# Kernel tuning notes

Hardware: AMD Instinct MI355X
Metric: run time of the kernel (lower is better)

The kernel has to match this reference:

```python
import jax, jax.numpy as jnp
import numpy as np

CROP_H, CROP_W = 14, 14


def _crop_and_resize_one_image(img, nboxes):
    """TF tf.image.crop_and_resize (bilinear, extrapolation_value=0) for one image.

    img: [H, W, C] float; nboxes: [N, 4] normalized (y1, x1, y2, x2).
    Returns [N, CROP_H, CROP_W, C].
    """
    H, W, C = img.shape
    dt = img.dtype
    y1, x1, y2, x2 = nboxes[:, 0], nboxes[:, 1], nboxes[:, 2], nboxes[:, 3]

    # Sample grid in pixel coordinates (crop size > 1 branch of TF op).
    ty = jnp.arange(CROP_H, dtype=dt) / (CROP_H - 1)  # [ch]
    tx = jnp.arange(CROP_W, dtype=dt) / (CROP_W - 1)  # [cw]
    ys = (y1[:, None] + (y2 - y1)[:, None] * ty[None, :]) * (H - 1)  # [N, ch]
    xs = (x1[:, None] + (x2 - x1)[:, None] * tx[None, :]) * (W - 1)  # [N, cw]

    valid_y = (ys >= 0) & (ys <= H - 1)  # [N, ch]
    valid_x = (xs >= 0) & (xs <= W - 1)  # [N, cw]

    y0f = jnp.floor(ys)
    x0f = jnp.floor(xs)
    wy = ys - y0f  # [N, ch]
    wx = xs - x0f  # [N, cw]
    y0 = jnp.clip(y0f, 0, H - 1).astype(jnp.int32)
    y1i = jnp.clip(y0f + 1, 0, H - 1).astype(jnp.int32)
    x0 = jnp.clip(x0f, 0, W - 1).astype(jnp.int32)
    x1i = jnp.clip(x0f + 1, 0, W - 1).astype(jnp.int32)

    def gather(yi, xi):  # yi [N,ch], xi [N,cw] -> [N,ch,cw,C]
        return img[yi[:, :, None], xi[:, None, :]]

    tl = gather(y0, x0)
    tr = gather(y0, x1i)
    bl = gather(y1i, x0)
    br = gather(y1i, x1i)

    wy_ = wy[:, :, None, None]
    wx_ = wx[:, None, :, None]
    out = (tl * (1 - wy_) * (1 - wx_) + tr * (1 - wy_) * wx_
           + bl * wy_ * (1 - wx_) + br * wy_ * wx_)

    mask = (valid_y[:, :, None] & valid_x[:, None, :])[..., None]
    return jnp.where(mask, out, jnp.zeros((), dtype=dt))


def setup_inputs() -> dict:
    key = jax.random.key(0)
    k1, k2, k3, k4, k5, k6 = jax.random.split(key, 6)
    B, N, H, W, C = 4, 256, 256, 256, 256
    # Boxes in pixel coordinates [x1, y1, x2, y2] with 0 <= x1 < x2 <= W etc.
    x1 = jax.random.uniform(k1, (B, N), minval=0.0, maxval=W / 2)
    y1 = jax.random.uniform(k2, (B, N), minval=0.0, maxval=H / 2)
    bw = jax.random.uniform(k3, (B, N), minval=4.0, maxval=W / 2)
    bh = jax.random.uniform(k4, (B, N), minval=4.0, maxval=H / 2)
    boxes = jnp.stack([x1, y1, x1 + bw, y1 + bh], axis=-1).astype(jnp.float32)
    fpn = jax.random.normal(k5, (B, H, W, C), dtype=jnp.float32)
    return {"boxes": boxes, "fpn": fpn}


def reference(boxes, fpn):
    boxes = jax.lax.stop_gradient(boxes)
    fpn = jax.lax.stop_gradient(fpn)
    B, H, W, C = fpn.shape
    Hf = jnp.asarray(H, dtype=fpn.dtype)
    Wf = jnp.asarray(W, dtype=fpn.dtype)

    x1 = boxes[..., 0]
    y1 = boxes[..., 1]
    x2 = boxes[..., 2]
    y2 = boxes[..., 3]
    # Exact normalization from the layer (image_shape == per-sample fpn shape).
    ny1 = y1 / Hf * Hf / (Hf - 1)
    nx1 = x1 / Wf * Wf / (Wf - 1)
    ny2 = (y2 / Hf * Hf - 1) / (Hf - 1)
    nx2 = (x2 / Wf * Wf - 1) / (Wf - 1)
    norm_boxes = jnp.stack([ny1, nx1, ny2, nx2], axis=-1)  # [B, N, 4]

    return jax.vmap(_crop_and_resize_one_image)(fpn, norm_boxes)
```

## Files before the change

### kernel.cpp

```cpp
#include <hip/hip_runtime.h>

constexpr int CROP_H = 14;
constexpr int CROP_W = 14;
constexpr int B = 4, N = 256, H = 256, W = 256, C = 256;
constexpr int C4 = C / 4;
constexpr int POSITIONS = B * N * CROP_H * CROP_W;
constexpr int NBOXES = B * N;
constexpr int ITEMS = NBOXES * CROP_H;
constexpr int NBINS = B * H;
constexpr int NXCD = 8;
constexpr int POS_PER_XCD = POSITIONS / NXCD;
constexpr size_t WS_NEEDED_BYTES = (size_t)ITEMS * 4;

typedef float vfloat4 __attribute__((ext_vector_type(4)));

__global__ __launch_bounds__(1024) void sort_rows_kernel(
    const float* __restrict__ boxes, unsigned int* __restrict__ perm) {
  __shared__ unsigned int cnt[NBINS];
  __shared__ unsigned int wsum[16];
  const int tid = threadIdx.x;
  cnt[tid] = 0u;
  __syncthreads();

  const float* bx = boxes + (size_t)tid * 4;
  const float y1 = bx[1], y2 = bx[3];
  const float Hf = (float)H;
  const float ny1 = y1 / Hf * Hf / (Hf - 1.0f);
  const float ny2 = (y2 / Hf * Hf - 1.0f) / (Hf - 1.0f);
  const int bimg = tid >> 8;

  unsigned int mybin[CROP_H];
#pragma unroll
  for (int i = 0; i < CROP_H; ++i) {
    float ty = (float)i / (float)(CROP_H - 1);
    float ys = (ny1 + (ny2 - ny1) * ty) * (Hf - 1.0f);
    float y0f = floorf(ys);
    int y0 = (int)fminf(fmaxf(y0f, 0.0f), Hf - 1.0f);
    mybin[i] = ((unsigned)bimg << 8) | (unsigned)y0;
    atomicAdd(&cnt[mybin[i]], 1u);
  }
  __syncthreads();

  unsigned c0 = cnt[tid];
  unsigned v = c0;
#pragma unroll
  for (int d = 1; d < 64; d <<= 1) {
    unsigned u = __shfl_up(v, d);
    if ((tid & 63) >= d) v += u;
  }
  if ((tid & 63) == 63) wsum[tid >> 6] = v;
  __syncthreads();
  if (tid == 0) {
    unsigned acc = 0;
    for (int w = 0; w < 16; ++w) { unsigned t = wsum[w]; wsum[w] = acc; acc += t; }
  }
  __syncthreads();
  cnt[tid] = v - c0 + wsum[tid >> 6];
  __syncthreads();

#pragma unroll
  for (int i = 0; i < CROP_H; ++i) {
    unsigned slot = atomicAdd(&cnt[mybin[i]], 1u);
    perm[slot] = (unsigned)(tid * CROP_H + i);
  }
}

template <bool USE_PERM>
__global__ __launch_bounds__(256) void roi_align_kernel(
    const float* __restrict__ boxes,
    const float* __restrict__ fpn,
    float* __restrict__ out,
    const unsigned int* __restrict__ perm) {
  const int wave = threadIdx.x >> 6;
  const int lane = threadIdx.x & 63;

  int pos;
  if (USE_PERM) {
    const int xcd = blockIdx.x & 7;
    const int r   = blockIdx.x >> 3;
    const unsigned slot = (unsigned)(xcd * POS_PER_XCD + r * 4 + wave);
    const unsigned it = slot / 14u;
    const unsigned jj = slot - it * 14u;
    pos = (int)(perm[it] * 14u + jj);
  } else {
    pos = blockIdx.x * 4 + wave;
  }

  int j = pos % CROP_W;
  int t = pos / CROP_W;
  int i = t % CROP_H;
  t /= CROP_H;
  int n = t % N;
  int b = t / N;

  const float* bx = boxes + (size_t)(b * N + n) * 4;
  float x1 = bx[0], y1 = bx[1], x2 = bx[2], y2 = bx[3];

  const float Hf = (float)H, Wf = (float)W;
  float ny1 = y1 / Hf * Hf / (Hf - 1.0f);
  float nx1 = x1 / Wf * Wf / (Wf - 1.0f);
  float ny2 = (y2 / Hf * Hf - 1.0f) / (Hf - 1.0f);
  float nx2 = (x2 / Wf * Wf - 1.0f) / (Wf - 1.0f);

  float ty = (float)i / (float)(CROP_H - 1);
  float tx = (float)j / (float)(CROP_W - 1);
  float ys = (ny1 + (ny2 - ny1) * ty) * (Hf - 1.0f);
  float xs = (nx1 + (nx2 - nx1) * tx) * (Wf - 1.0f);

  bool valid = (ys >= 0.0f) && (ys <= Hf - 1.0f) &&
               (xs >= 0.0f) && (xs <= Wf - 1.0f);

  float y0f = floorf(ys), x0f = floorf(xs);
  float wy = ys - y0f, wx = xs - x0f;
  int y0  = (int)fminf(fmaxf(y0f,        0.0f), Hf - 1.0f);
  int y1i = (int)fminf(fmaxf(y0f + 1.0f, 0.0f), Hf - 1.0f);
  int x0  = (int)fminf(fmaxf(x0f,        0.0f), Wf - 1.0f);
  int x1i = (int)fminf(fmaxf(x0f + 1.0f, 0.0f), Wf - 1.0f);

  const float4* f4 = (const float4*)fpn;
  int rb = b * H;
  size_t i00 = (size_t)((rb + y0)  * W + x0)  * C4 + lane;
  size_t i01 = (size_t)((rb + y0)  * W + x1i) * C4 + lane;
  size_t i10 = (size_t)((rb + y1i) * W + x0)  * C4 + lane;
  size_t i11 = (size_t)((rb + y1i) * W + x1i) * C4 + lane;

  float4 tl = f4[i00];
  float4 tr = f4[i01];
  float4 bl = f4[i10];
  float4 br = f4[i11];

  float w00 = (1.0f - wy) * (1.0f - wx);
  float w01 = (1.0f - wy) * wx;
  float w10 = wy * (1.0f - wx);
  float w11 = wy * wx;

  vfloat4 o;
  o.x = tl.x * w00 + tr.x * w01 + bl.x * w10 + br.x * w11;
  o.y = tl.y * w00 + tr.y * w01 + bl.y * w10 + br.y * w11;
  o.z = tl.z * w00 + tr.z * w01 + bl.z * w10 + br.z * w11;
  o.w = tl.w * w00 + tr.w * w01 + bl.w * w10 + br.w * w11;
  if (!valid) { o.x = 0.0f; o.y = 0.0f; o.z = 0.0f; o.w = 0.0f; }

  vfloat4* dst = (vfloat4*)out + (size_t)pos * C4 + lane;
  __builtin_nontemporal_store(o, dst);
}

extern "C" void kernel_launch(void* const* d_in, const int* in_sizes, int n_in,
                              void* d_out, int out_size, void* d_ws, size_t ws_size,
                              hipStream_t stream) {
  const float* boxes = (const float*)d_in[0];
  const float* fpn   = (const float*)d_in[1];
  float* out = (float*)d_out;

  if (d_ws != nullptr && ws_size >= WS_NEEDED_BYTES) {
    unsigned int* perm = (unsigned int*)d_ws;
    hipLaunchKernelGGL(sort_rows_kernel, dim3(1), dim3(1024), 0, stream,
                       boxes, perm);
    hipLaunchKernelGGL(roi_align_kernel<true>, dim3(POSITIONS / 4), dim3(256),
                       0, stream, boxes, fpn, out, perm);
  } else {
    hipLaunchKernelGGL(roi_align_kernel<false>, dim3(POSITIONS / 4), dim3(256),
                       0, stream, boxes, fpn, out, (const unsigned int*)nullptr);
  }
}
```

Before: 430.7 us.

## Add cooperative software prefetch of upcoming feature rows and per-image row sort

The row-bucket sort now runs as one block per image and writes bin start offsets into the workspace alongside the permutation. Each wave in the main kernel uses those offsets to work out its position within its row bucket, then loads a share of the feature row two rows ahead, which warms cache for the waves that follow. The loaded values are kept live only through an empty asm statement. This adds extra global loads and index arithmetic per wave in exchange for fewer cache misses on later rows.

```diff
diff --git a/kernel.cpp b/kernel.cpp
--- a/kernel.cpp
+++ b/kernel.cpp
@@ -5,29 +5,30 @@
 constexpr int B = 4, N = 256, H = 256, W = 256, C = 256;
 constexpr int C4 = C / 4;
 constexpr int POSITIONS = B * N * CROP_H * CROP_W;
-constexpr int NBOXES = B * N;
-constexpr int ITEMS = NBOXES * CROP_H;
-constexpr int NBINS = B * H;
+constexpr int ITEMS_PER_IMG = N * CROP_H;
+constexpr int ITEMS = B * ITEMS_PER_IMG;
+constexpr int ROW_F4 = W * C4;
 constexpr int NXCD = 8;
 constexpr int POS_PER_XCD = POSITIONS / NXCD;
-constexpr size_t WS_NEEDED_BYTES = (size_t)ITEMS * 4;
+constexpr int WS_PERM = 1056;
+constexpr size_t WS_NEEDED_BYTES = (size_t)(WS_PERM + ITEMS) * 4;
 
 typedef float vfloat4 __attribute__((ext_vector_type(4)));
 
-__global__ __launch_bounds__(1024) void sort_rows_kernel(
-    const float* __restrict__ boxes, unsigned int* __restrict__ perm) {
-  __shared__ unsigned int cnt[NBINS];
-  __shared__ unsigned int wsum[16];
+__global__ __launch_bounds__(256) void sort_rows_kernel(
+    const float* __restrict__ boxes, unsigned int* __restrict__ ws) {
+  __shared__ unsigned int cnt[256];
+  __shared__ unsigned int wsum[4];
+  const int b = blockIdx.x;
   const int tid = threadIdx.x;
   cnt[tid] = 0u;
   __syncthreads();
 
-  const float* bx = boxes + (size_t)tid * 4;
+  const float* bx = boxes + (size_t)(b * N + tid) * 4;
   const float y1 = bx[1], y2 = bx[3];
   const float Hf = (float)H;
   const float ny1 = y1 / Hf * Hf / (Hf - 1.0f);
   const float ny2 = (y2 / Hf * Hf - 1.0f) / (Hf - 1.0f);
-  const int bimg = tid >> 8;
 
   unsigned int mybin[CROP_H];
 #pragma unroll
@@ -36,8 +37,8 @@
     float ys = (ny1 + (ny2 - ny1) * ty) * (Hf - 1.0f);
     float y0f = floorf(ys);
     int y0 = (int)fminf(fmaxf(y0f, 0.0f), Hf - 1.0f);
-    mybin[i] = ((unsigned)bimg << 8) | (unsigned)y0;
-    atomicAdd(&cnt[mybin[i]], 1u);
+    mybin[i] = (unsigned)y0;
+    atomicAdd(&cnt[y0], 1u);
   }
   __syncthreads();
 
@@ -52,16 +53,20 @@
   __syncthreads();
   if (tid == 0) {
     unsigned acc = 0;
-    for (int w = 0; w < 16; ++w) { unsigned t = wsum[w]; wsum[w] = acc; acc += t; }
+    for (int w = 0; w < 4; ++w) { unsigned t = wsum[w]; wsum[w] = acc; acc += t; }
   }
   __syncthreads();
-  cnt[tid] = v - c0 + wsum[tid >> 6];
+  const unsigned start = v - c0 + wsum[tid >> 6];
+  ws[(b << 8) | tid] = (unsigned)(b * ITEMS_PER_IMG) + start;
+  if (b == 3 && tid == 0) ws[1024] = (unsigned)ITEMS;
+  cnt[tid] = start;
   __syncthreads();
 
 #pragma unroll
   for (int i = 0; i < CROP_H; ++i) {
     unsigned slot = atomicAdd(&cnt[mybin[i]], 1u);
-    perm[slot] = (unsigned)(tid * CROP_H + i);
+    ws[WS_PERM + b * ITEMS_PER_IMG + slot] =
+        (unsigned)((b * N + tid) * CROP_H + i);
   }
 }
 
@@ -70,18 +75,19 @@
     const float* __restrict__ boxes,
     const float* __restrict__ fpn,
     float* __restrict__ out,
-    const unsigned int* __restrict__ perm) {
+    const unsigned int* __restrict__ ws) {
   const int wave = threadIdx.x >> 6;
   const int lane = threadIdx.x & 63;
 
   int pos;
+  int slot = 0;
   if (USE_PERM) {
     const int xcd = blockIdx.x & 7;
     const int r   = blockIdx.x >> 3;
-    const unsigned slot = (unsigned)(xcd * POS_PER_XCD + r * 4 + wave);
-    const unsigned it = slot / 14u;
-    const unsigned jj = slot - it * 14u;
-    pos = (int)(perm[it] * 14u + jj);
+    slot = xcd * POS_PER_XCD + r * 4 + wave;
+    const unsigned it = (unsigned)slot / 14u;
+    const unsigned jj = (unsigned)slot - it * 14u;
+    pos = (int)(ws[WS_PERM + it] * 14u + jj);
   } else {
     pos = blockIdx.x * 4 + wave;
   }
@@ -119,6 +125,30 @@
 
   const float4* f4 = (const float4*)fpn;
   int rb = b * H;
+
+  if (USE_PERM) {
+    const unsigned bin = ((unsigned)b << 8) | (unsigned)y0;
+    const unsigned o0 = ws[bin];
+    const unsigned o1 = ws[bin + 1];
+    const int s_pos = (int)(o1 - o0) * 14;
+    const int q = slot - (int)o0 * 14;
+    int share = (256 + s_pos - 1) / s_pos;
+    if (share > 4) share = 4;
+    const int rowt = (y0 + 2 <= H - 1) ? (y0 + 2) : (H - 1);
+    const float4* rowbase = f4 + (size_t)(rb + rowt) * ROW_F4;
+    const int kb0 = q * share;
+    float acc = 0.0f;
+    if (kb0 < 256) {
+      for (int l = 0; l < share; ++l) {
+        if (kb0 + l < 256) {
+          float4 v = rowbase[(size_t)(kb0 + l) * 64 + lane];
+          acc += v.x;
+        }
+      }
+    }
+    asm volatile("" :: "v"(acc));
+  }
+
   size_t i00 = (size_t)((rb + y0)  * W + x0)  * C4 + lane;
   size_t i01 = (size_t)((rb + y0)  * W + x1i) * C4 + lane;
   size_t i10 = (size_t)((rb + y1i) * W + x0)  * C4 + lane;
@@ -153,11 +183,11 @@
   float* out = (float*)d_out;
 
   if (d_ws != nullptr && ws_size >= WS_NEEDED_BYTES) {
-    unsigned int* perm = (unsigned int*)d_ws;
-    hipLaunchKernelGGL(sort_rows_kernel, dim3(1), dim3(1024), 0, stream,
-                       boxes, perm);
+    unsigned int* ws = (unsigned int*)d_ws;
+    hipLaunchKernelGGL(sort_rows_kernel, dim3(B), dim3(256), 0, stream,
+                       boxes, ws);
     hipLaunchKernelGGL(roi_align_kernel<true>, dim3(POSITIONS / 4), dim3(256),
-                       0, stream, boxes, fpn, out, perm);
+                       0, stream, boxes, fpn, out, ws);
   } else {
     hipLaunchKernelGGL(roi_align_kernel<false>, dim3(POSITIONS / 4), dim3(256),
                        0, stream, boxes, fpn, out, (const unsigned int*)nullptr);
```

Result: slower. 461.1 us (+7.1%).
